# Performance work log

Hardware: AMD Instinct MI355X
Metric: run time of the kernel (lower is better)

The kernel has to match this reference:

```python
import jax, jax.numpy as jnp
import numpy as np

V, E, H, O, L = 32000, 512, 512, 32, 2
B, T = 64, 512


def setup_inputs() -> dict:
    key = jax.random.key(0)
    ks = jax.random.split(key, 10)
    s = 0.02
    x = jax.random.randint(ks[0], (B, T), 0, V, dtype=jnp.int64)
    seq_lens = jax.random.randint(ks[1], (B,), 1, T + 1, dtype=jnp.int64)
    emb = jax.random.normal(ks[2], (V, E), dtype=jnp.float32) * s
    Whx = jax.random.normal(ks[3], (L, H, E), dtype=jnp.float32) * s  # [out,in] like nn.Linear
    Whh = jax.random.normal(ks[4], (L, H, H), dtype=jnp.float32) * s
    b_h = jnp.zeros((L, H), dtype=jnp.float32)
    Wyh = jax.random.normal(ks[5], (L, H, H), dtype=jnp.float32) * s
    b_y = jnp.zeros((L, H), dtype=jnp.float32)
    Wf = jax.random.normal(ks[6], (O, H), dtype=jnp.float32) * s
    bf = jnp.zeros((O,), dtype=jnp.float32)
    return {"x": x, "sequence_lengths": seq_lens, "emb": emb, "Whx": Whx,
            "Whh": Whh, "b_h": b_h, "Wyh": Wyh, "b_y": b_y, "Wf": Wf, "bf": bf}


def reference(x, sequence_lengths, emb, Whx, Whh, b_h, Wyh, b_y, Wf, bf):
    Bsz, Tlen = x.shape
    x_emb = emb[x]                      # [B,T,E]
    xs = jnp.swapaxes(x_emb, 0, 1)      # time-major [T,B,E]
    h0 = jnp.zeros((L, Bsz, H), dtype=x_emb.dtype)

    def step(h, xt):
        inp = xt
        hs = []
        for l in range(L):
            hl = jnp.tanh(inp @ Whx[l].T + h[l] @ Whh[l].T + b_h[l])
            hs.append(hl)
            inp = hl
        # only the last layer's y is kept by the original loop
        y = inp @ Wyh[L - 1].T + b_y[L - 1]
        return jnp.stack(hs), y

    _, outputs = jax.lax.scan(step, h0, xs)     # outputs: [T,B,H]
    outputs = jnp.swapaxes(outputs, 0, 1)       # [B,T,H]
    idx = sequence_lengths - 1                  # last valid timestep per example
    final_hidden = outputs[jnp.arange(Bsz), idx]  # [B,H]
    return final_hidden @ Wf.T + bf             # [B,O]
```

## Files before the change

kernel.cpp:

```cpp
#include <hip/hip_runtime.h>

namespace {
constexpr int E_ = 512;
constexpr int H_ = 512;
constexpr int O_ = 32;
constexpr int B_ = 64;
constexpr int T_ = 512;
constexpr int RING = 8;
constexpr int FPAD = 16;
constexpr size_t H0_OFF   = 0;
constexpr size_t H1_OFF   = (size_t)RING * B_ * H_;
constexpr size_t HF_OFF   = 2 * H1_OFF;
constexpr size_t FLAG_OFF = HF_OFF + (size_t)B_ * H_;
constexpr size_t FLAG_UINTS = 2u * 8u * 16u * FPAD;
constexpr size_t WS_REQUIRED = (FLAG_OFF + FLAG_UINTS) * 4;
}

typedef float f32x4 __attribute__((ext_vector_type(4)));

__device__ __forceinline__ void ring_issue4(const float* p, f32x4& a, f32x4& b,
                                            f32x4& c, f32x4& d) {
    asm volatile(
        "global_load_dwordx4 %0, %4, off sc0 sc1\n\t"
        "global_load_dwordx4 %1, %4, off offset:1024 sc0 sc1\n\t"
        "global_load_dwordx4 %2, %4, off offset:2048 sc0 sc1\n\t"
        "global_load_dwordx4 %3, %4, off offset:3072 sc0 sc1"
        : "=&v"(a), "=&v"(b), "=&v"(c), "=&v"(d)
        : "v"(p) : "memory");
}
__device__ __forceinline__ void vm_drain() {
    asm volatile("s_waitcnt vmcnt(0)" ::: "memory");
}
__device__ __forceinline__ void coh_store(float* p, float v) {
    asm volatile("global_store_dword %0, %1, off sc0 sc1" :: "v"(p), "v"(v) : "memory");
}
__device__ __forceinline__ void flag_store(unsigned* p, unsigned v) {
    asm volatile("global_store_dword %0, %1, off sc0 sc1" :: "v"(p), "v"(v) : "memory");
}
__device__ __forceinline__ unsigned flag_load(const unsigned* p) {
    unsigned v;
    asm volatile("global_load_dword %0, %1, off sc0 sc1\n\ts_waitcnt vmcnt(0)"
                 : "=&v"(v) : "v"(p) : "memory");
    return v;
}

__device__ __forceinline__ float fast_tanh(float x) {
    float e = __builtin_amdgcn_exp2f(x * 2.885390081777927f);
    return 1.0f - 2.0f * __builtin_amdgcn_rcpf(e + 1.0f);
}

__device__ __forceinline__ float reduce8(const float v[8], int lane) {
    float a[4];
#pragma unroll
    for (int j = 0; j < 4; ++j) {
        const int sel = lane & 1;
        const float mine = sel ? v[2 * j + 1] : v[2 * j];
        const float send = sel ? v[2 * j] : v[2 * j + 1];
        a[j] = mine + __shfl_xor(send, 1, 64);
    }
    float b[2];
#pragma unroll
    for (int j = 0; j < 2; ++j) {
        const int sel = (lane >> 1) & 1;
        const float mine = sel ? a[2 * j + 1] : a[2 * j];
        const float send = sel ? a[2 * j] : a[2 * j + 1];
        b[j] = mine + __shfl_xor(send, 2, 64);
    }
    const int sel = (lane >> 2) & 1;
    const float mine = sel ? b[1] : b[0];
    const float send = sel ? b[0] : b[1];
    float s = mine + __shfl_xor(send, 4, 64);
    s += __shfl_xor(s, 8, 64);
    s += __shfl_xor(s, 16, 64);
    s += __shfl_xor(s, 32, 64);
    return s;
}

__global__ __launch_bounds__(512, 2) void rnn_pipe2(
    const int* __restrict__ x, const int* __restrict__ seq_lens,
    const float* __restrict__ emb,
    const float* __restrict__ Whx, const float* __restrict__ Whh,
    const float* __restrict__ b_h,
    float* __restrict__ h0_ring, float* __restrict__ h1_ring,
    float* __restrict__ h1_final, unsigned* __restrict__ flags)
{
    const int bid   = blockIdx.x;
    const int layer = bid >> 7;
    const int g     = (bid >> 4) & 7;
    const int c     = bid & 15;
    const int tid   = threadIdx.x;
    const int wid   = tid >> 6;
    const int lane  = tid & 63;
    const int wr    = wid & 3;
    const int we    = wid >> 2;
    const int rowbase = c * 32 + wr * 8;

    __shared__ float sx[2][4096];

    const float* WxL = Whx + (size_t)layer * H_ * E_;
    const float* WhL = Whh + (size_t)layer * H_ * H_;
    float w[8][16];
#pragma unroll
    for (int r = 0; r < 8; ++r) {
        const int row = rowbase + r;
        const f32x4 x0 = *(const f32x4*)(WxL + (size_t)row * E_ + (lane << 2));
        const f32x4 x1 = *(const f32x4*)(WxL + (size_t)row * E_ + 256 + (lane << 2));
        const f32x4 h0 = *(const f32x4*)(WhL + (size_t)row * H_ + (lane << 2));
        const f32x4 h1 = *(const f32x4*)(WhL + (size_t)row * H_ + 256 + (lane << 2));
#pragma unroll
        for (int m = 0; m < 4; ++m) {
            w[r][m] = x0[m]; w[r][4 + m] = x1[m];
            w[r][8 + m] = h0[m]; w[r][12 + m] = h1[m];
        }
    }
    const float bias = b_h[layer * H_ + rowbase + (lane & 7)];

    int sl4[4];
#pragma unroll
    for (int q = 0; q < 4; ++q) sl4[q] = seq_lens[(g << 3) + (we << 2) + q];
    int Tg = 1;
#pragma unroll
    for (int j = 0; j < 8; ++j) {
        const int s = seq_lens[(g << 3) + j];
        Tg = s > Tg ? s : Tg;
    }

    unsigned* const f0 = flags;
    unsigned* const f1 = flags + 128 * FPAD;
    unsigned* const myflag = (layer == 0 ? f0 : f1) + ((g << 4) + c) * FPAD;
    const unsigned* pollp = f0;
    int which = 0;
    if (wid == 0) {
        if (lane < 16)      { pollp = f0 + ((g << 4) + lane) * FPAD;        which = 1; }
        else if (lane < 32) { pollp = f1 + ((g << 4) + (lane - 16)) * FPAD; which = 2; }
    }

    const int se  = tid >> 6;
    const int seg = (g << 3) + se;

    if (layer == 0) {
        const int tok = x[(size_t)seg * T_];
        const f32x4* er = (const f32x4*)(emb + ((size_t)tok << 9) + (lane << 2));
        *(f32x4*)&sx[0][(se << 9) + (lane << 2)]       = er[0];
        *(f32x4*)&sx[0][(se << 9) + 256 + (lane << 2)] = er[64];
    }

    const int egbase = (g << 3) + (we << 2);
    long spin_budget = 1l << 27;

    for (int t = 0; t < Tg; ++t) {
        const int slot  = t & (RING - 1);
        const int pslot = (t - 1) & (RING - 1);

        {
            int tA, tB;
            if (layer == 0) { tA = t;     tB = t - (RING - 1); }
            else            { tA = t + 1; tB = t; }
            const unsigned uA = tA > 0 ? (unsigned)tA : 0u;
            const unsigned uB = tB > 0 ? (unsigned)tB : 0u;
            if (wid == 0 && (uA | uB)) {
                for (;;) {
                    const unsigned fv = flag_load(pollp);
                    const bool bad = (which == 1 && fv < uA) || (which == 2 && fv < uB);
                    if (!__any(bad)) break;
                    if (--spin_budget < 0) break;
                    __builtin_amdgcn_s_sleep(1);
                }
            }
        }
        __syncthreads();

        f32x4 xr[4][2], hr[4][2];
        if (layer == 1) {
            const float* px = h0_ring + (((size_t)slot << 6) + egbase) * 512 + (lane << 2);
            ring_issue4(px,        xr[0][0], xr[0][1], xr[1][0], xr[1][1]);
            ring_issue4(px + 1024, xr[2][0], xr[2][1], xr[3][0], xr[3][1]);
            if (t > 0) {
                const float* ph = h1_ring + (((size_t)pslot << 6) + egbase) * 512 + (lane << 2);
                ring_issue4(ph,        hr[0][0], hr[0][1], hr[1][0], hr[1][1]);
                ring_issue4(ph + 1024, hr[2][0], hr[2][1], hr[3][0], hr[3][1]);
            } else {
#pragma unroll
                for (int q = 0; q < 4; ++q) { hr[q][0] = 0; hr[q][1] = 0; }
            }
        } else {
            if (t > 0) {
                const float* ph = h0_ring + (((size_t)pslot << 6) + egbase) * 512 + (lane << 2);
                ring_issue4(ph,        hr[0][0], hr[0][1], hr[1][0], hr[1][1]);
                ring_issue4(ph + 1024, hr[2][0], hr[2][1], hr[3][0], hr[3][1]);
            } else {
#pragma unroll
                for (int q = 0; q < 4; ++q) { hr[q][0] = 0; hr[q][1] = 0; }
            }
        }
        vm_drain();
        __builtin_amdgcn_sched_barrier(0);

        f32x4 pf0, pf1;
        const bool havepf = (layer == 0) && (t + 1 < Tg);
        if (havepf) {
            const int tok = x[(size_t)seg * T_ + t + 1];
            const f32x4* er = (const f32x4*)(emb + ((size_t)tok << 9) + (lane << 2));
            pf0 = er[0]; pf1 = er[64];
        }

        float* const oring = (layer == 0) ? h0_ring : h1_ring;
#pragma unroll
        for (int q = 0; q < 4; ++q) {
            const int slq = sl4[q];
            if (t >= slq) continue;
            const int el = (we << 2) + q;
            const int eg = egbase + q;

            float A[16];
            if (layer == 0) {
                const f32x4 lx0 = *(const f32x4*)&sx[t & 1][(el << 9) + (lane << 2)];
                const f32x4 lx1 = *(const f32x4*)&sx[t & 1][(el << 9) + 256 + (lane << 2)];
#pragma unroll
                for (int m = 0; m < 4; ++m) { A[m] = lx0[m]; A[4 + m] = lx1[m]; }
            } else {
#pragma unroll
                for (int m = 0; m < 4; ++m) { A[m] = xr[q][0][m]; A[4 + m] = xr[q][1][m]; }
            }
#pragma unroll
            for (int m = 0; m < 4; ++m) { A[8 + m] = hr[q][0][m]; A[12 + m] = hr[q][1][m]; }

            float vv[8];
#pragma unroll
            for (int r = 0; r < 8; ++r) {
                float s = w[r][0] * A[0];
#pragma unroll
                for (int j = 1; j < 16; ++j) s = fmaf(w[r][j], A[j], s);
                vv[r] = s;
            }
            const float sum = reduce8(vv, lane);
            const float hv = fast_tanh(sum + bias);
            if (lane < 8) {
                coh_store(oring + (((size_t)slot << 6) + eg) * 512 + rowbase + lane, hv);
                if (layer == 1 && t == slq - 1)
                    h1_final[((size_t)eg << 9) + rowbase + lane] = hv;
            }
        }

        if (havepf) {
            *(f32x4*)&sx[(t + 1) & 1][(se << 9) + (lane << 2)]       = pf0;
            *(f32x4*)&sx[(t + 1) & 1][(se << 9) + 256 + (lane << 2)] = pf1;
        }

        vm_drain();
        __syncthreads();
        if (tid == 0) flag_store(myflag, (unsigned)(t + 1));
    }
}

__device__ __forceinline__ float dot4(float4 a, float4 b) {
    return fmaf(a.x, b.x, fmaf(a.y, b.y, fmaf(a.z, b.z, a.w * b.w)));
}
__device__ __forceinline__ float wave_reduce(float acc) {
#pragma unroll
    for (int off = 32; off > 0; off >>= 1) acc += __shfl_down(acc, off, 64);
    return acc;
}

__global__ __launch_bounds__(512) void head_kernel(
    const float* __restrict__ h1f, const float* __restrict__ Wyh,
    const float* __restrict__ b_y, const float* __restrict__ Wf,
    const float* __restrict__ bf, float* __restrict__ out)
{
    const int e = blockIdx.x;
    const int tid = threadIdx.x, wid = tid >> 6, lane = tid & 63;
    const int k0 = lane << 3;
    __shared__ float sh[H_];
    __shared__ float sy[H_];
    sh[tid] = h1f[(size_t)e * H_ + tid];
    __syncthreads();
    const float4 hA = *(const float4*)&sh[k0];
    const float4 hB = *(const float4*)&sh[k0 + 4];
    const float* Wy1 = Wyh + H_ * H_;
#pragma unroll 4
    for (int rr = 0; rr < 64; ++rr) {
        const int row = (wid << 6) + rr;
        float acc = wave_reduce(dot4(*(const float4*)&Wy1[(size_t)row * H_ + k0], hA) +
                                dot4(*(const float4*)&Wy1[(size_t)row * H_ + k0 + 4], hB));
        if (lane == 0) sy[row] = acc + b_y[H_ + row];
    }
    __syncthreads();
    const float4 yA = *(const float4*)&sy[k0];
    const float4 yB = *(const float4*)&sy[k0 + 4];
#pragma unroll
    for (int rr = 0; rr < 4; ++rr) {
        const int o = (wid << 2) + rr;
        float acc = wave_reduce(dot4(*(const float4*)&Wf[(size_t)o * H_ + k0], yA) +
                                dot4(*(const float4*)&Wf[(size_t)o * H_ + k0 + 4], yB));
        if (lane == 0) out[(size_t)e * O_ + o] = acc + bf[o];
    }
}

__global__ __launch_bounds__(1024, 1) void rnn_fused_fb(
    const int* __restrict__ x, const int* __restrict__ seq_lens,
    const float* __restrict__ emb, const float* __restrict__ Whx,
    const float* __restrict__ Whh, const float* __restrict__ b_h,
    const float* __restrict__ Wyh, const float* __restrict__ b_y,
    const float* __restrict__ Wf, const float* __restrict__ bf,
    float* __restrict__ out)
{
    const int b = blockIdx.x, tid = threadIdx.x;
    const int wave = tid >> 6, lane = tid & 63, k0 = lane << 3;
    __shared__ float s_inp[E_];
    __shared__ float s_h0[2][H_];
    __shared__ float s_h1[2][H_];
    __shared__ float s_y[H_];
    if (tid < H_) { s_h0[0][tid]=0.f; s_h0[1][tid]=0.f; s_h1[0][tid]=0.f; s_h1[1][tid]=0.f; }
    const int Tb = seq_lens[b];
    const float* Whx0 = Whx; const float* Whx1 = Whx + H_*E_;
    const float* Whh0 = Whh; const float* Whh1 = Whh + H_*H_;
    for (int t = 0; t < Tb; ++t) {
        const int cur = t & 1, prv = cur ^ 1;
        if (tid < E_) { const int tok = x[b*T_+t]; s_inp[tid] = emb[(size_t)tok*E_+tid]; }
        __syncthreads();
        const float4 iA = *(const float4*)&s_inp[k0], iB = *(const float4*)&s_inp[k0+4];
        const float4 pA = *(const float4*)&s_h0[prv][k0], pB = *(const float4*)&s_h0[prv][k0+4];
#pragma unroll 4
        for (int r = 0; r < 32; ++r) {
            const int i = (wave<<5)+r;
            float acc = dot4(*(const float4*)&Whx0[i*E_+k0], iA) + dot4(*(const float4*)&Whx0[i*E_+k0+4], iB)
                      + dot4(*(const float4*)&Whh0[i*H_+k0], pA) + dot4(*(const float4*)&Whh0[i*H_+k0+4], pB);
            acc = wave_reduce(acc);
            if (lane == 0) s_h0[cur][i] = tanhf(acc + b_h[i]);
        }
        __syncthreads();
        const float4 cA = *(const float4*)&s_h0[cur][k0], cB = *(const float4*)&s_h0[cur][k0+4];
        const float4 qA = *(const float4*)&s_h1[prv][k0], qB = *(const float4*)&s_h1[prv][k0+4];
#pragma unroll 4
        for (int r = 0; r < 32; ++r) {
            const int i = (wave<<5)+r;
            float acc = dot4(*(const float4*)&Whx1[i*E_+k0], cA) + dot4(*(const float4*)&Whx1[i*E_+k0+4], cB)
                      + dot4(*(const float4*)&Whh1[i*H_+k0], qA) + dot4(*(const float4*)&Whh1[i*H_+k0+4], qB);
            acc = wave_reduce(acc);
            if (lane == 0) s_h1[cur][i] = tanhf(acc + b_h[H_+i]);
        }
        __syncthreads();
    }
    const int lastb = (Tb-1) & 1;
    const float4 hA = *(const float4*)&s_h1[lastb][k0], hB = *(const float4*)&s_h1[lastb][k0+4];
    const float* Wy1 = Wyh + H_*H_;
#pragma unroll 4
    for (int r = 0; r < 32; ++r) {
        const int i = (wave<<5)+r;
        float acc = wave_reduce(dot4(*(const float4*)&Wy1[i*H_+k0], hA) + dot4(*(const float4*)&Wy1[i*H_+k0+4], hB));
        if (lane == 0) s_y[i] = acc + b_y[H_+i];
    }
    __syncthreads();
    const float4 yA = *(const float4*)&s_y[k0], yB = *(const float4*)&s_y[k0+4];
    if (wave < 8) {
#pragma unroll
        for (int r = 0; r < 4; ++r) {
            const int o = (wave<<2)+r;
            float acc = wave_reduce(dot4(*(const float4*)&Wf[o*H_+k0], yA) + dot4(*(const float4*)&Wf[o*H_+k0+4], yB));
            if (lane == 0) out[b*O_+o] = acc + bf[o];
        }
    }
}

extern "C" void kernel_launch(void* const* d_in, const int* in_sizes, int n_in,
                              void* d_out, int out_size, void* d_ws, size_t ws_size,
                              hipStream_t stream) {
    const int*   x    = (const int*)d_in[0];
    const int*   sl   = (const int*)d_in[1];
    const float* emb  = (const float*)d_in[2];
    const float* Whx  = (const float*)d_in[3];
    const float* Whh  = (const float*)d_in[4];
    const float* b_h  = (const float*)d_in[5];
    const float* Wyh  = (const float*)d_in[6];
    const float* b_y  = (const float*)d_in[7];
    const float* Wf   = (const float*)d_in[8];
    const float* bf   = (const float*)d_in[9];
    float* out = (float*)d_out;

    if (ws_size < WS_REQUIRED) {
        rnn_fused_fb<<<B_, 1024, 0, stream>>>(x, sl, emb, Whx, Whh, b_h, Wyh, b_y, Wf, bf, out);
        return;
    }

    float* ws_f = (float*)d_ws;
    float* h0_ring = ws_f + H0_OFF;
    float* h1_ring = ws_f + H1_OFF;
    float* h1f     = ws_f + HF_OFF;
    unsigned* flags = (unsigned*)(ws_f + FLAG_OFF);

    hipMemsetAsync(flags, 0, FLAG_UINTS * sizeof(unsigned), stream);
    rnn_pipe2<<<256, 512, 0, stream>>>(x, sl, emb, Whx, Whh, b_h,
                                       h0_ring, h1_ring, h1f, flags);
    head_kernel<<<B_, 512, 0, stream>>>(h1f, Wyh, b_y, Wf, bf, out);
}
```

Baseline: 2.207 ms.

## Split RNN recurrence per layer, precompute input projection before flag wait, stage hidden state in LDS

The persistent pipelined RNN kernel now has separate loops for layer 0 and layer 1. Layer 0 computes the embedding-input half of its dot products before polling the inter-block flags, so that work overlaps the wait. Hidden-state rows are fetched cooperatively with one coherent load per thread into shared memory, then read from LDS, instead of each wave issuing its own strided global loads. The trade-off is extra LDS, more barriers per step, launch bounds relaxed to one block per SM, no sleep in the spin loop and a smaller spin budget, which risks hangs or a silent fallthrough if a producer runs slow.

```diff
diff --git a/kernel.cpp b/kernel.cpp
--- a/kernel.cpp
+++ b/kernel.cpp
@@ -18,30 +18,37 @@
 
 typedef float f32x4 __attribute__((ext_vector_type(4)));
 
-__device__ __forceinline__ void ring_issue4(const float* p, f32x4& a, f32x4& b,
-                                            f32x4& c, f32x4& d) {
+__device__ __forceinline__ void coh_ld8(const float* p, f32x4& a, f32x4& b) {
+    asm volatile(
+        "global_load_dwordx4 %0, %2, off sc0 sc1\n\t"
+        "global_load_dwordx4 %1, %2, off offset:16 sc0 sc1\n\t"
+        "s_waitcnt vmcnt(0)"
+        : "=&v"(a), "=&v"(b) : "v"(p) : "memory");
+}
+__device__ __forceinline__ void coh_ld16(const float* p, const float* q,
+                                         f32x4& a, f32x4& b, f32x4& c, f32x4& d) {
     asm volatile(
         "global_load_dwordx4 %0, %4, off sc0 sc1\n\t"
-        "global_load_dwordx4 %1, %4, off offset:1024 sc0 sc1\n\t"
-        "global_load_dwordx4 %2, %4, off offset:2048 sc0 sc1\n\t"
-        "global_load_dwordx4 %3, %4, off offset:3072 sc0 sc1"
-        : "=&v"(a), "=&v"(b), "=&v"(c), "=&v"(d)
-        : "v"(p) : "memory");
-}
-__device__ __forceinline__ void vm_drain() {
-    asm volatile("s_waitcnt vmcnt(0)" ::: "memory");
-}
-__device__ __forceinline__ void coh_store(float* p, float v) {
-    asm volatile("global_store_dword %0, %1, off sc0 sc1" :: "v"(p), "v"(v) : "memory");
-}
-__device__ __forceinline__ void flag_store(unsigned* p, unsigned v) {
-    asm volatile("global_store_dword %0, %1, off sc0 sc1" :: "v"(p), "v"(v) : "memory");
-}
-__device__ __forceinline__ unsigned flag_load(const unsigned* p) {
+        "global_load_dwordx4 %1, %4, off offset:16 sc0 sc1\n\t"
+        "global_load_dwordx4 %2, %5, off sc0 sc1\n\t"
+        "global_load_dwordx4 %3, %5, off offset:16 sc0 sc1\n\t"
+        "s_waitcnt vmcnt(0)"
+        : "=&v"(a), "=&v"(b), "=&v"(c), "=&v"(d) : "v"(p), "v"(q) : "memory");
+}
+__device__ __forceinline__ unsigned flag_poll(const unsigned* p) {
     unsigned v;
     asm volatile("global_load_dword %0, %1, off sc0 sc1\n\ts_waitcnt vmcnt(0)"
                  : "=&v"(v) : "v"(p) : "memory");
     return v;
+}
+__device__ __forceinline__ void vm_drain() {
+    asm volatile("s_waitcnt vmcnt(0)" ::: "memory");
+}
+__device__ __forceinline__ void coh_store(float* p, float v) {
+    asm volatile("global_store_dword %0, %1, off sc0 sc1" :: "v"(p), "v"(v) : "memory");
+}
+__device__ __forceinline__ void flag_store(unsigned* p, unsigned v) {
+    asm volatile("global_store_dword %0, %1, off sc0 sc1" :: "v"(p), "v"(v) : "memory");
 }
 
 __device__ __forceinline__ float fast_tanh(float x) {
@@ -76,7 +83,7 @@
     return s;
 }
 
-__global__ __launch_bounds__(512, 2) void rnn_pipe2(
+__global__ __launch_bounds__(512, 1) void rnn_pipe6(
     const int* __restrict__ x, const int* __restrict__ seq_lens,
     const float* __restrict__ emb,
     const float* __restrict__ Whx, const float* __restrict__ Whh,
@@ -91,11 +98,14 @@
     const int tid   = threadIdx.x;
     const int wid   = tid >> 6;
     const int lane  = tid & 63;
+    const int we    = wid >> 2;
     const int wr    = wid & 3;
-    const int we    = wid >> 2;
     const int rowbase = c * 32 + wr * 8;
+    const int eg0   = g * 8 + we * 4;
 
     __shared__ float sx[2][4096];
+    __shared__ float sh[4096];
+    __shared__ float sh1[4096];
 
     const float* WxL = Whx + (size_t)layer * H_ * E_;
     const float* WhL = Whh + (size_t)layer * H_ * H_;
@@ -117,139 +127,194 @@
 
     int sl4[4];
 #pragma unroll
-    for (int q = 0; q < 4; ++q) sl4[q] = seq_lens[(g << 3) + (we << 2) + q];
+    for (int q = 0; q < 4; ++q) sl4[q] = seq_lens[eg0 + q];
     int Tg = 1;
 #pragma unroll
     for (int j = 0; j < 8; ++j) {
-        const int s = seq_lens[(g << 3) + j];
+        const int s = seq_lens[g * 8 + j];
         Tg = s > Tg ? s : Tg;
     }
 
-    unsigned* const f0 = flags;
-    unsigned* const f1 = flags + 128 * FPAD;
-    unsigned* const myflag = (layer == 0 ? f0 : f1) + ((g << 4) + c) * FPAD;
-    const unsigned* pollp = f0;
-    int which = 0;
-    if (wid == 0) {
-        if (lane < 16)      { pollp = f0 + ((g << 4) + lane) * FPAD;        which = 1; }
-        else if (lane < 32) { pollp = f1 + ((g << 4) + (lane - 16)) * FPAD; which = 2; }
-    }
-
-    const int se  = tid >> 6;
-    const int seg = (g << 3) + se;
+    unsigned* const myflag = flags + ((size_t)((layer * 8 + g) * 16 + c)) * FPAD;
+    const unsigned* pollp = flags + ((size_t)((0 * 8 + g) * 16 + (lane & 15))) * FPAD;
+    if (lane >= 16 && lane < 32)
+        pollp = flags + ((size_t)((8 + g) * 16 + (lane - 16))) * FPAD;
+
+    const int se  = wid;
+    const int off = (tid & 63) << 3;
+    const int seg = g * 8 + se;
+
+    long budget = 1l << 24;
 
     if (layer == 0) {
-        const int tok = x[(size_t)seg * T_];
-        const f32x4* er = (const f32x4*)(emb + ((size_t)tok << 9) + (lane << 2));
-        *(f32x4*)&sx[0][(se << 9) + (lane << 2)]       = er[0];
-        *(f32x4*)&sx[0][(se << 9) + 256 + (lane << 2)] = er[64];
-    }
-
-    const int egbase = (g << 3) + (we << 2);
-    long spin_budget = 1l << 27;
-
-    for (int t = 0; t < Tg; ++t) {
-        const int slot  = t & (RING - 1);
-        const int pslot = (t - 1) & (RING - 1);
-
         {
-            int tA, tB;
-            if (layer == 0) { tA = t;     tB = t - (RING - 1); }
-            else            { tA = t + 1; tB = t; }
-            const unsigned uA = tA > 0 ? (unsigned)tA : 0u;
-            const unsigned uB = tB > 0 ? (unsigned)tB : 0u;
-            if (wid == 0 && (uA | uB)) {
+            const int tok = x[(size_t)seg * T_];
+            const f32x4 e0 = *(const f32x4*)(emb + ((size_t)tok << 9) + off);
+            const f32x4 e1 = *(const f32x4*)(emb + ((size_t)tok << 9) + off + 4);
+            *(f32x4*)&sx[0][(se << 9) + off] = e0;
+            *(f32x4*)&sx[0][(se << 9) + off + 4] = e1;
+        }
+        __syncthreads();
+
+        for (int t = 0; t < Tg; ++t) {
+            const int cur = t & 1, slot = t & 7, pslot = (t - 1) & 7;
+            float vvp[4][8];
+
+#pragma unroll
+            for (int q = 0; q < 4; ++q) {
+                if (t >= sl4[q]) continue;
+                const int el = (we << 2) + q;
+                const f32x4 lx0 = *(const f32x4*)&sx[cur][(el << 9) + (lane << 2)];
+                const f32x4 lx1 = *(const f32x4*)&sx[cur][(el << 9) + 256 + (lane << 2)];
+#pragma unroll
+                for (int r = 0; r < 8; ++r) {
+                    float s = w[r][0] * lx0[0];
+                    s = fmaf(w[r][1], lx0[1], s);
+                    s = fmaf(w[r][2], lx0[2], s);
+                    s = fmaf(w[r][3], lx0[3], s);
+                    s = fmaf(w[r][4], lx1[0], s);
+                    s = fmaf(w[r][5], lx1[1], s);
+                    s = fmaf(w[r][6], lx1[2], s);
+                    s = fmaf(w[r][7], lx1[3], s);
+                    vvp[q][r] = s;
+                }
+            }
+
+            if (wid == 0 && t > 0) {
+                const int tgt = (lane < 16) ? t : ((lane < 32) ? t - 7 : 0);
                 for (;;) {
-                    const unsigned fv = flag_load(pollp);
-                    const bool bad = (which == 1 && fv < uA) || (which == 2 && fv < uB);
-                    if (!__any(bad)) break;
-                    if (--spin_budget < 0) break;
-                    __builtin_amdgcn_s_sleep(1);
-                }
-            }
-        }
-        __syncthreads();
-
-        f32x4 xr[4][2], hr[4][2];
-        if (layer == 1) {
-            const float* px = h0_ring + (((size_t)slot << 6) + egbase) * 512 + (lane << 2);
-            ring_issue4(px,        xr[0][0], xr[0][1], xr[1][0], xr[1][1]);
-            ring_issue4(px + 1024, xr[2][0], xr[2][1], xr[3][0], xr[3][1]);
+                    const unsigned v = flag_poll(pollp);
+                    if (!__any((int)v < tgt)) break;
+                    if (--budget < 0) break;
+                }
+            }
+            __syncthreads();
+
             if (t > 0) {
-                const float* ph = h1_ring + (((size_t)pslot << 6) + egbase) * 512 + (lane << 2);
-                ring_issue4(ph,        hr[0][0], hr[0][1], hr[1][0], hr[1][1]);
-                ring_issue4(ph + 1024, hr[2][0], hr[2][1], hr[3][0], hr[3][1]);
+                f32x4 a, b;
+                coh_ld8(h0_ring + (((size_t)pslot << 6) + seg) * 512 + off, a, b);
+                *(f32x4*)&sh[(se << 9) + off] = a;
+                *(f32x4*)&sh[(se << 9) + off + 4] = b;
             } else {
-#pragma unroll
-                for (int q = 0; q < 4; ++q) { hr[q][0] = 0; hr[q][1] = 0; }
-            }
-        } else {
+                f32x4 z = 0;
+                *(f32x4*)&sh[(se << 9) + off] = z;
+                *(f32x4*)&sh[(se << 9) + off + 4] = z;
+            }
+            f32x4 px0, px1;
+            const bool havepf = (t + 1 < Tg);
+            if (havepf) {
+                const int tok = x[(size_t)seg * T_ + t + 1];
+                px0 = *(const f32x4*)(emb + ((size_t)tok << 9) + off);
+                px1 = *(const f32x4*)(emb + ((size_t)tok << 9) + off + 4);
+            }
+            __syncthreads();
+
+#pragma unroll
+            for (int q = 0; q < 4; ++q) {
+                if (t >= sl4[q]) continue;
+                const int el = (we << 2) + q;
+                const f32x4 h0a = *(const f32x4*)&sh[(el << 9) + (lane << 2)];
+                const f32x4 h0b = *(const f32x4*)&sh[(el << 9) + 256 + (lane << 2)];
+#pragma unroll
+                for (int r = 0; r < 8; ++r) {
+                    float s = vvp[q][r];
+                    s = fmaf(w[r][8],  h0a[0], s);
+                    s = fmaf(w[r][9],  h0a[1], s);
+                    s = fmaf(w[r][10], h0a[2], s);
+                    s = fmaf(w[r][11], h0a[3], s);
+                    s = fmaf(w[r][12], h0b[0], s);
+                    s = fmaf(w[r][13], h0b[1], s);
+                    s = fmaf(w[r][14], h0b[2], s);
+                    s = fmaf(w[r][15], h0b[3], s);
+                    vvp[q][r] = s;
+                }
+                const float sum = reduce8(vvp[q], lane);
+                const float hv = fast_tanh(sum + bias);
+                if (lane < 8)
+                    coh_store(h0_ring + (((size_t)slot << 6) + eg0 + q) * 512 + rowbase + lane, hv);
+            }
+            if (havepf) {
+                *(f32x4*)&sx[cur ^ 1][(se << 9) + off] = px0;
+                *(f32x4*)&sx[cur ^ 1][(se << 9) + off + 4] = px1;
+            }
+            vm_drain();
+            __syncthreads();
+            if (tid == 0) flag_store(myflag, (unsigned)(t + 1));
+        }
+    } else {
+        for (int t = 0; t < Tg; ++t) {
+            const int slot = t & 7, pslot = (t - 1) & 7;
+            float vvp[4][8];
+
+            if (wid == 0) {
+                const int tgt = (lane < 16) ? t + 1 : ((lane < 32) ? t : 0);
+                for (;;) {
+                    const unsigned v = flag_poll(pollp);
+                    if (!__any((int)v < tgt)) break;
+                    if (--budget < 0) break;
+                }
+            }
+            __syncthreads();
+
             if (t > 0) {
-                const float* ph = h0_ring + (((size_t)pslot << 6) + egbase) * 512 + (lane << 2);
-                ring_issue4(ph,        hr[0][0], hr[0][1], hr[1][0], hr[1][1]);
-                ring_issue4(ph + 1024, hr[2][0], hr[2][1], hr[3][0], hr[3][1]);
+                f32x4 a, b, cc, d;
+                coh_ld16(h0_ring + (((size_t)slot << 6) + seg) * 512 + off,
+                         h1_ring + (((size_t)pslot << 6) + seg) * 512 + off, a, b, cc, d);
+                *(f32x4*)&sh[(se << 9) + off] = a;
+                *(f32x4*)&sh[(se << 9) + off + 4] = b;
+                *(f32x4*)&sh1[(se << 9) + off] = cc;
+                *(f32x4*)&sh1[(se << 9) + off + 4] = d;
             } else {
-#pragma unroll
-                for (int q = 0; q < 4; ++q) { hr[q][0] = 0; hr[q][1] = 0; }
-            }
-        }
-        vm_drain();
-        __builtin_amdgcn_sched_barrier(0);
-
-        f32x4 pf0, pf1;
-        const bool havepf = (layer == 0) && (t + 1 < Tg);
-        if (havepf) {
-            const int tok = x[(size_t)seg * T_ + t + 1];
-            const f32x4* er = (const f32x4*)(emb + ((size_t)tok << 9) + (lane << 2));
-            pf0 = er[0]; pf1 = er[64];
-        }
-
-        float* const oring = (layer == 0) ? h0_ring : h1_ring;
-#pragma unroll
-        for (int q = 0; q < 4; ++q) {
-            const int slq = sl4[q];
-            if (t >= slq) continue;
-            const int el = (we << 2) + q;
-            const int eg = egbase + q;
-
-            float A[16];
-            if (layer == 0) {
-                const f32x4 lx0 = *(const f32x4*)&sx[t & 1][(el << 9) + (lane << 2)];
-                const f32x4 lx1 = *(const f32x4*)&sx[t & 1][(el << 9) + 256 + (lane << 2)];
-#pragma unroll
-                for (int m = 0; m < 4; ++m) { A[m] = lx0[m]; A[4 + m] = lx1[m]; }
-            } else {
-#pragma unroll
-                for (int m = 0; m < 4; ++m) { A[m] = xr[q][0][m]; A[4 + m] = xr[q][1][m]; }
-            }
-#pragma unroll
-            for (int m = 0; m < 4; ++m) { A[8 + m] = hr[q][0][m]; A[12 + m] = hr[q][1][m]; }
-
-            float vv[8];
-#pragma unroll
-            for (int r = 0; r < 8; ++r) {
-                float s = w[r][0] * A[0];
-#pragma unroll
-                for (int j = 1; j < 16; ++j) s = fmaf(w[r][j], A[j], s);
-                vv[r] = s;
-            }
-            const float sum = reduce8(vv, lane);
-            const float hv = fast_tanh(sum + bias);
-            if (lane < 8) {
-                coh_store(oring + (((size_t)slot << 6) + eg) * 512 + rowbase + lane, hv);
-                if (layer == 1 && t == slq - 1)
-                    h1_final[((size_t)eg << 9) + rowbase + lane] = hv;
-            }
-        }
-
-        if (havepf) {
-            *(f32x4*)&sx[(t + 1) & 1][(se << 9) + (lane << 2)]       = pf0;
-            *(f32x4*)&sx[(t + 1) & 1][(se << 9) + 256 + (lane << 2)] = pf1;
-        }
-
-        vm_drain();
-        __syncthreads();
-        if (tid == 0) flag_store(myflag, (unsigned)(t + 1));
+                f32x4 a, b;
+                coh_ld8(h0_ring + (((size_t)slot << 6) + seg) * 512 + off, a, b);
+                *(f32x4*)&sh[(se << 9) + off] = a;
+                *(f32x4*)&sh[(se << 9) + off + 4] = b;
+                f32x4 z = 0;
+                *(f32x4*)&sh1[(se << 9) + off] = z;
+                *(f32x4*)&sh1[(se << 9) + off + 4] = z;
+            }
+            __syncthreads();
+
+#pragma unroll
+            for (int q = 0; q < 4; ++q) {
+                if (t >= sl4[q]) continue;
+                const int el = (we << 2) + q;
+                const f32x4 xa = *(const f32x4*)&sh[(el << 9) + (lane << 2)];
+                const f32x4 xb = *(const f32x4*)&sh[(el << 9) + 256 + (lane << 2)];
+                const f32x4 ha = *(const f32x4*)&sh1[(el << 9) + (lane << 2)];
+                const f32x4 hb = *(const f32x4*)&sh1[(el << 9) + 256 + (lane << 2)];
+#pragma unroll
+                for (int r = 0; r < 8; ++r) {
+                    float s = w[r][0] * xa[0];
+                    s = fmaf(w[r][1], xa[1], s);
+                    s = fmaf(w[r][2], xa[2], s);
+                    s = fmaf(w[r][3], xa[3], s);
+                    s = fmaf(w[r][4], xb[0], s);
+                    s = fmaf(w[r][5], xb[1], s);
+                    s = fmaf(w[r][6], xb[2], s);
+                    s = fmaf(w[r][7], xb[3], s);
+                    s = fmaf(w[r][8],  ha[0], s);
+                    s = fmaf(w[r][9],  ha[1], s);
+                    s = fmaf(w[r][10], ha[2], s);
+                    s = fmaf(w[r][11], ha[3], s);
+                    s = fmaf(w[r][12], hb[0], s);
+                    s = fmaf(w[r][13], hb[1], s);
+                    s = fmaf(w[r][14], hb[2], s);
+                    s = fmaf(w[r][15], hb[3], s);
+                    vvp[q][r] = s;
+                }
+                const float sum = reduce8(vvp[q], lane);
+                const float hv = fast_tanh(sum + bias);
+                if (lane < 8) {
+                    coh_store(h1_ring + (((size_t)slot << 6) + eg0 + q) * 512 + rowbase + lane, hv);
+                    if (t == sl4[q] - 1)
+                        h1_final[((size_t)(eg0 + q) << 9) + rowbase + lane] = hv;
+                }
+            }
+            vm_drain();
+            __syncthreads();
+            if (tid == 0) flag_store(myflag, (unsigned)(t + 1));
+        }
     }
 }
 
@@ -389,7 +454,7 @@
     unsigned* flags = (unsigned*)(ws_f + FLAG_OFF);
 
     hipMemsetAsync(flags, 0, FLAG_UINTS * sizeof(unsigned), stream);
-    rnn_pipe2<<<256, 512, 0, stream>>>(x, sl, emb, Whx, Whh, b_h,
+    rnn_pipe6<<<256, 512, 0, stream>>>(x, sl, emb, Whx, Whh, b_h,
                                        h0_ring, h1_ring, h1f, flags);
     head_kernel<<<B_, 512, 0, stream>>>(h1f, Wyh, b_y, Wf, bf, out);
 }
```

After: 1.991 ms. 9.8% less time.
